# Kernel optimization log

Hardware: AMD Instinct MI355X
Metric: run time of the kernel (lower is better)

## Reference

```python
import jax, jax.numpy as jnp
import numpy as np

B, F, C = 16384, 256, 256


def setup_inputs() -> dict:
    key = jax.random.key(0)
    ks = jax.random.split(key, 10)
    return {
        "x_t": jax.random.normal(ks[0], (B, F), dtype=jnp.float32),
        "n_t": jax.random.normal(ks[1], (B, C), dtype=jnp.float32),
        "d_t": jax.random.uniform(ks[2], (B, C), dtype=jnp.float32),
        "h_t": jax.random.normal(ks[3], (B, C), dtype=jnp.float32),
        "a_max_t": jax.random.normal(ks[4], (B, C), dtype=jnp.float32),
        "Wu": jax.random.normal(ks[5], (C, F), dtype=jnp.float32) * 0.06,
        "bu": jnp.zeros((C,), dtype=jnp.float32),
        "Wg": jax.random.normal(ks[6], (C, F + C), dtype=jnp.float32) * 0.05,
        "bg": jnp.zeros((C,), dtype=jnp.float32),
        "Wa": jax.random.normal(ks[7], (C, F + C), dtype=jnp.float32) * 0.05,
        "Wd": jax.random.normal(ks[8], (C, F + C), dtype=jnp.float32) * 0.05,
    }


def reference(x_t, n_t, d_t, h_t, a_max_t, Wu, bu, Wg, bg, Wa, Wd):
    # xh_join = cat([x_t, h_t], dim=1) -> [B, F+C]
    xh = jnp.concatenate([x_t, h_t], axis=1)
    u_t = x_t @ Wu.T + bu                      # [B, C]
    g_t = xh @ Wg.T + bg                       # [B, C]
    a_t = xh @ Wa.T                            # [B, C] (no bias)
    z_t = u_t * jnp.tanh(g_t)
    # decay branch (self.decay is an nn.Linear -> always truthy in original)
    decay = jax.nn.sigmoid(xh @ Wd.T)
    e_neg = jnp.exp(-decay)
    a_decay = a_max_t * e_neg
    a_newmax = jnp.maximum(a_decay, a_t)
    exp_diff = jnp.exp(a_max_t - a_newmax)
    exp_scaled = jnp.exp(a_t - a_newmax)
    n_new = n_t * e_neg * exp_diff + z_t * exp_scaled
    d_new = d_t * e_neg * exp_diff + exp_scaled
    h_new = jnp.tanh(n_new / d_new)
    return (n_new, d_new, h_new, a_newmax)
```

## Files before the change

### kernel.cpp

```cpp
#include <hip/hip_runtime.h>
#include <stdint.h>

typedef _Float16 f16x8 __attribute__((ext_vector_type(8)));
typedef __fp16 fp16x2 __attribute__((ext_vector_type(2)));
typedef float f32x4 __attribute__((ext_vector_type(4)));

#define BC (16384 * 256)

__device__ __forceinline__ f16x8 cvt8(f32x4 a, f32x4 b) {
  fp16x2 p0 = __builtin_amdgcn_cvt_pkrtz(a[0], a[1]);
  fp16x2 p1 = __builtin_amdgcn_cvt_pkrtz(a[2], a[3]);
  fp16x2 p2 = __builtin_amdgcn_cvt_pkrtz(b[0], b[1]);
  fp16x2 p3 = __builtin_amdgcn_cvt_pkrtz(b[2], b[3]);
  f16x8 o;
  o[0] = (_Float16)p0[0]; o[1] = (_Float16)p0[1];
  o[2] = (_Float16)p1[0]; o[3] = (_Float16)p1[1];
  o[4] = (_Float16)p2[0]; o[5] = (_Float16)p2[1];
  o[6] = (_Float16)p3[0]; o[7] = (_Float16)p3[1];
  return o;
}

__device__ __forceinline__ float tanh_fast(float v) {
  float a = fminf(fabsf(v), 18.f);
  float t = __expf(2.f * a);
  float r = (t - 1.f) * __builtin_amdgcn_rcpf(t + 1.f);
  return copysignf(r, v);
}

__global__ __launch_bounds__(256) void pack_w(const float* __restrict__ Wu,
                                              const float* __restrict__ Wg,
                                              const float* __restrict__ Wa,
                                              const float* __restrict__ Wd,
                                              _Float16* __restrict__ wsB) {
  int tid = blockIdx.x * 256 + threadIdx.x;
  int slot = tid & 3;
  int row = (tid >> 2) & 127;
  int cb = (tid >> 9) & 7;
  int kt = tid >> 12;
  int strip = (row >> 4) & 3;
  int wn = row >> 6;
  int t16 = row & 15;
  int c = cb * 32 + wn * 16 + t16;
  int k0 = kt * 32 + (slot ^ ((row >> 1) & 3)) * 8;
  float v[8];
  if (strip == 0) {
    if (k0 < 256) {
      const float* p = Wu + (size_t)c * 256 + k0;
#pragma unroll
      for (int i = 0; i < 8; ++i) v[i] = p[i];
    } else {
#pragma unroll
      for (int i = 0; i < 8; ++i) v[i] = 0.f;
    }
  } else {
    const float* p = (strip == 1 ? Wg : (strip == 2 ? Wa : Wd)) + (size_t)c * 512 + k0;
#pragma unroll
    for (int i = 0; i < 8; ++i) v[i] = p[i];
  }
  f32x4 a = {v[0], v[1], v[2], v[3]};
  f32x4 b = {v[4], v[5], v[6], v[7]};
  *reinterpret_cast<f16x8*>(wsB + (size_t)tid * 8) = cvt8(a, b);
}

__global__ __launch_bounds__(256, 6) void rwa_main(
    const float* __restrict__ x, const float* __restrict__ nt_,
    const float* __restrict__ dt_, const float* __restrict__ h,
    const float* __restrict__ amax_, const float* __restrict__ bu,
    const float* __restrict__ bg, const _Float16* __restrict__ wsB,
    float* __restrict__ out) {
  __shared__ __align__(16) _Float16 ldsA[2][64 * 32];
  __shared__ __align__(16) _Float16 ldsB[2][128 * 32];

  const int tid = threadIdx.x;
  const int lane = tid & 63;
  const int l15 = lane & 15;
  const int lg = lane >> 4;
  const int wv = tid >> 6;
  const int wm = wv & 1;
  const int wn = wv >> 1;

  const int bid = blockIdx.x;
  const int xcd = bid & 7;
  const int q = bid >> 3;
  const int cb = q & 7;
  const int rowblk = xcd * 32 + (q >> 3);
  const int row0 = rowblk * 64;

  const int ar = tid >> 2;
  const int aq = tid & 3;
  const int awoff = ar * 64 + ((aq ^ ((ar >> 1) & 3)) << 4);

  const _Float16* bsrc0 = wsB + (size_t)cb * 4096 + (size_t)tid * 8;

  f32x4 acc[2][4] = {};
  f32x4 a0, a1;

  auto issueA = [&](int kt) {
    const float* sp = (kt < 8 ? x : h) + (size_t)(row0 + ar) * 256 + (kt & 7) * 32 + aq * 8;
    a0 = *reinterpret_cast<const f32x4*>(sp);
    a1 = *reinterpret_cast<const f32x4*>(sp + 4);
  };
  auto issueB = [&](int buf, int kt) {
#pragma unroll
    for (int i = 0; i < 2; ++i) {
      __builtin_amdgcn_global_load_lds(
          (const __attribute__((address_space(1))) uint32_t*)(bsrc0 + (size_t)kt * 32768 + i * 2048),
          (__attribute__((address_space(3))) uint32_t*)(&ldsB[buf][0] + wv * 512 + i * 2048),
          16, 0, 0);
    }
  };
  auto writeA = [&](int buf) {
    *reinterpret_cast<f16x8*>(reinterpret_cast<char*>(&ldsA[buf][0]) + awoff) = cvt8(a0, a1);
  };

  issueA(0);
  issueB(0, 0);
  writeA(0);

#pragma unroll
  for (int kt = 0; kt < 16; ++kt) {
    const int buf = kt & 1;
    if (kt < 15) {
      issueA(kt + 1);
      issueB(buf ^ 1, kt + 1);
    }

    if (kt < 15) {
      asm volatile("s_waitcnt vmcnt(4) lgkmcnt(0)" ::: "memory");
    } else {
      asm volatile("s_waitcnt vmcnt(0) lgkmcnt(0)" ::: "memory");
    }
    __builtin_amdgcn_s_barrier();
    __builtin_amdgcn_sched_barrier(0);

    const bool doU = (kt < 8);
    const char* pA = reinterpret_cast<const char*>(&ldsA[buf][0]);
    const char* pB = reinterpret_cast<const char*>(&ldsB[buf][0]);
    {
      f16x8 af[2], bf[4];
#pragma unroll
      for (int mi = 0; mi < 2; ++mi) {
        const int row = wm * 32 + mi * 16 + l15;
        af[mi] = *reinterpret_cast<const f16x8*>(pA + row * 64 + ((lg ^ ((row >> 1) & 3)) << 4));
      }
#pragma unroll
      for (int s = 0; s < 4; ++s) {
        if (s == 0 && !doU) continue;
        const int pc = wn * 64 + s * 16 + l15;
        bf[s] = *reinterpret_cast<const f16x8*>(pB + pc * 64 + ((lg ^ ((pc >> 1) & 3)) << 4));
      }
#pragma unroll
      for (int s = 0; s < 4; ++s) {
        if (s == 0 && !doU) continue;
#pragma unroll
        for (int mi = 0; mi < 2; ++mi)
          acc[mi][s] = __builtin_amdgcn_mfma_f32_16x16x32_f16(af[mi], bf[s], acc[mi][s], 0, 0, 0);
      }
    }

    if (kt < 15) {
      writeA(buf ^ 1);
      asm volatile("s_waitcnt lgkmcnt(0)" ::: "memory");
      __builtin_amdgcn_s_barrier();
      __builtin_amdgcn_sched_barrier(0);
    }
  }

  __builtin_amdgcn_sched_barrier(0);

  const int c = cb * 32 + wn * 16 + l15;
  const float buv = bu[c];
  const float bgv = bg[c];
#pragma unroll
  for (int mi = 0; mi < 2; ++mi) {
#pragma unroll
    for (int rg = 0; rg < 4; ++rg) {
      const int r = row0 + wm * 32 + mi * 16 + lg * 4 + rg;
      const int idx = r * 256 + c;
      const float u = acc[mi][0][rg] + buv;
      const float gt = acc[mi][1][rg] + bgv;
      const float a = acc[mi][2][rg];
      const float dr = acc[mi][3][rg];
      const float sig = __builtin_amdgcn_rcpf(1.f + __expf(-dr));
      const float z = u * tanh_fast(gt);
      const float am = amax_[idx];
      const float n_old = nt_[idx];
      const float d_old = dt_[idx];
      const float e_neg = __expf(-sig);
      const float a_new = fmaxf(am * e_neg, a);
      const float comm = __expf(am - a_new - sig);
      const float escal = __expf(a - a_new);
      const float n_new = n_old * comm + z * escal;
      const float d_new = d_old * comm + escal;
      const float h_new = tanh_fast(n_new * __builtin_amdgcn_rcpf(d_new));
      out[idx] = n_new;
      out[BC + idx] = d_new;
      out[2 * BC + idx] = h_new;
      out[3 * BC + idx] = a_new;
    }
  }
}

extern "C" void kernel_launch(void* const* d_in, const int* in_sizes, int n_in,
                              void* d_out, int out_size, void* d_ws, size_t ws_size,
                              hipStream_t stream) {
  const float* x_t    = (const float*)d_in[0];
  const float* n_t    = (const float*)d_in[1];
  const float* d_t    = (const float*)d_in[2];
  const float* h_t    = (const float*)d_in[3];
  const float* amax_t = (const float*)d_in[4];
  const float* Wu     = (const float*)d_in[5];
  const float* bu     = (const float*)d_in[6];
  const float* Wg     = (const float*)d_in[7];
  const float* bg     = (const float*)d_in[8];
  const float* Wa     = (const float*)d_in[9];
  const float* Wd     = (const float*)d_in[10];
  float* out = (float*)d_out;

  _Float16* wsB = (_Float16*)d_ws;

  pack_w<<<256, 256, 0, stream>>>(Wu, Wg, Wa, Wd, wsB);
  rwa_main<<<2048, 256, 0, stream>>>(x_t, n_t, d_t, h_t, amax_t, bu, bg, wsB, out);
}
```

Measured before the change: 46.52 us.

## Use single-wave blocks loading A fragments directly from global into registers

Restructures the main kernel from 4-wave 64x128 tiles to 1-wave blocks computing 32 rows by 16 output columns across all four gate strips. The activation fragments are now loaded straight from global memory into MFMA register layout, so the LDS staging for A and all block barriers go away. The packed weight layout is reordered to match. The cost is less reuse: each activation row is re-read by 16 column blocks instead of 8, and the grid grows to 8192 small blocks.

Measured after the change: 89.41 us. +92.2%, slower.

```diff
diff --git a/kernel.cpp b/kernel.cpp
--- a/kernel.cpp
+++ b/kernel.cpp
@@ -34,16 +34,14 @@
                                               _Float16* __restrict__ wsB) {
   int tid = blockIdx.x * 256 + threadIdx.x;
   int slot = tid & 3;
-  int row = (tid >> 2) & 127;
-  int cb = (tid >> 9) & 7;
-  int kt = tid >> 12;
-  int strip = (row >> 4) & 3;
-  int wn = row >> 6;
-  int t16 = row & 15;
-  int c = cb * 32 + wn * 16 + t16;
-  int k0 = kt * 32 + (slot ^ ((row >> 1) & 3)) * 8;
+  int pr = (tid >> 2) & 63;
+  int kt = (tid >> 8) & 15;
+  int cbh = tid >> 12;
+  int s = pr >> 4;
+  int c = cbh * 16 + (pr & 15);
+  int k0 = kt * 32 + (slot ^ ((pr >> 1) & 3)) * 8;
   float v[8];
-  if (strip == 0) {
+  if (s == 0) {
     if (k0 < 256) {
       const float* p = Wu + (size_t)c * 256 + k0;
 #pragma unroll
@@ -53,7 +51,7 @@
       for (int i = 0; i < 8; ++i) v[i] = 0.f;
     }
   } else {
-    const float* p = (strip == 1 ? Wg : (strip == 2 ? Wa : Wd)) + (size_t)c * 512 + k0;
+    const float* p = (s == 1 ? Wg : (s == 2 ? Wa : Wd)) + (size_t)c * 512 + k0;
 #pragma unroll
     for (int i = 0; i < 8; ++i) v[i] = p[i];
   }
@@ -62,120 +60,102 @@
   *reinterpret_cast<f16x8*>(wsB + (size_t)tid * 8) = cvt8(a, b);
 }
 
-__global__ __launch_bounds__(256, 6) void rwa_main(
+__global__ __launch_bounds__(64, 4) void rwa_main(
     const float* __restrict__ x, const float* __restrict__ nt_,
     const float* __restrict__ dt_, const float* __restrict__ h,
     const float* __restrict__ amax_, const float* __restrict__ bu,
     const float* __restrict__ bg, const _Float16* __restrict__ wsB,
     float* __restrict__ out) {
-  __shared__ __align__(16) _Float16 ldsA[2][64 * 32];
-  __shared__ __align__(16) _Float16 ldsB[2][128 * 32];
-
-  const int tid = threadIdx.x;
-  const int lane = tid & 63;
+  __shared__ __align__(16) _Float16 ldsB[2][64 * 32];
+
+  const int lane = threadIdx.x;
   const int l15 = lane & 15;
   const int lg = lane >> 4;
-  const int wv = tid >> 6;
-  const int wm = wv & 1;
-  const int wn = wv >> 1;
 
   const int bid = blockIdx.x;
   const int xcd = bid & 7;
   const int q = bid >> 3;
-  const int cb = q & 7;
-  const int rowblk = xcd * 32 + (q >> 3);
-  const int row0 = rowblk * 64;
-
-  const int ar = tid >> 2;
-  const int aq = tid & 3;
-  const int awoff = ar * 64 + ((aq ^ ((ar >> 1) & 3)) << 4);
-
-  const _Float16* bsrc0 = wsB + (size_t)cb * 4096 + (size_t)tid * 8;
+  const int cbh = q & 15;
+  const int r32 = xcd * 64 + (q >> 4);
+  const int row0 = r32 * 32;
+
+  const float* xr0 = x + (size_t)(row0 + l15) * 256 + lg * 8;
+  const float* hr0 = h + (size_t)(row0 + l15) * 256 + lg * 8;
+  const float* xr1 = xr0 + 16 * 256;
+  const float* hr1 = hr0 + 16 * 256;
+
+  const _Float16* bslab = wsB + (size_t)cbh * 32768 + (size_t)lane * 8;
 
   f32x4 acc[2][4] = {};
-  f32x4 a0, a1;
+  f32x4 a0, a1, a2, a3;
 
   auto issueA = [&](int kt) {
-    const float* sp = (kt < 8 ? x : h) + (size_t)(row0 + ar) * 256 + (kt & 7) * 32 + aq * 8;
-    a0 = *reinterpret_cast<const f32x4*>(sp);
-    a1 = *reinterpret_cast<const f32x4*>(sp + 4);
+    const float* p0 = (kt < 8 ? xr0 : hr0) + (kt & 7) * 32;
+    const float* p1 = (kt < 8 ? xr1 : hr1) + (kt & 7) * 32;
+    a0 = *reinterpret_cast<const f32x4*>(p0);
+    a1 = *reinterpret_cast<const f32x4*>(p0 + 4);
+    a2 = *reinterpret_cast<const f32x4*>(p1);
+    a3 = *reinterpret_cast<const f32x4*>(p1 + 4);
   };
   auto issueB = [&](int buf, int kt) {
 #pragma unroll
-    for (int i = 0; i < 2; ++i) {
+    for (int i = 0; i < 4; ++i) {
       __builtin_amdgcn_global_load_lds(
-          (const __attribute__((address_space(1))) uint32_t*)(bsrc0 + (size_t)kt * 32768 + i * 2048),
-          (__attribute__((address_space(3))) uint32_t*)(&ldsB[buf][0] + wv * 512 + i * 2048),
+          (const __attribute__((address_space(1))) uint32_t*)(bslab + (size_t)kt * 2048 + i * 512),
+          (__attribute__((address_space(3))) uint32_t*)(&ldsB[buf][0] + i * 512),
           16, 0, 0);
     }
-  };
-  auto writeA = [&](int buf) {
-    *reinterpret_cast<f16x8*>(reinterpret_cast<char*>(&ldsA[buf][0]) + awoff) = cvt8(a0, a1);
   };
 
   issueA(0);
   issueB(0, 0);
-  writeA(0);
 
 #pragma unroll
   for (int kt = 0; kt < 16; ++kt) {
     const int buf = kt & 1;
+
+    f16x8 af0 = cvt8(a0, a1);
+    f16x8 af1 = cvt8(a2, a3);
+
     if (kt < 15) {
       issueA(kt + 1);
       issueB(buf ^ 1, kt + 1);
     }
 
     if (kt < 15) {
-      asm volatile("s_waitcnt vmcnt(4) lgkmcnt(0)" ::: "memory");
+      asm volatile("s_waitcnt vmcnt(8)" ::: "memory");
     } else {
-      asm volatile("s_waitcnt vmcnt(0) lgkmcnt(0)" ::: "memory");
-    }
-    __builtin_amdgcn_s_barrier();
+      asm volatile("s_waitcnt vmcnt(0)" ::: "memory");
+    }
     __builtin_amdgcn_sched_barrier(0);
 
     const bool doU = (kt < 8);
-    const char* pA = reinterpret_cast<const char*>(&ldsA[buf][0]);
     const char* pB = reinterpret_cast<const char*>(&ldsB[buf][0]);
-    {
-      f16x8 af[2], bf[4];
-#pragma unroll
-      for (int mi = 0; mi < 2; ++mi) {
-        const int row = wm * 32 + mi * 16 + l15;
-        af[mi] = *reinterpret_cast<const f16x8*>(pA + row * 64 + ((lg ^ ((row >> 1) & 3)) << 4));
-      }
-#pragma unroll
-      for (int s = 0; s < 4; ++s) {
-        if (s == 0 && !doU) continue;
-        const int pc = wn * 64 + s * 16 + l15;
-        bf[s] = *reinterpret_cast<const f16x8*>(pB + pc * 64 + ((lg ^ ((pc >> 1) & 3)) << 4));
-      }
-#pragma unroll
-      for (int s = 0; s < 4; ++s) {
-        if (s == 0 && !doU) continue;
-#pragma unroll
-        for (int mi = 0; mi < 2; ++mi)
-          acc[mi][s] = __builtin_amdgcn_mfma_f32_16x16x32_f16(af[mi], bf[s], acc[mi][s], 0, 0, 0);
-      }
-    }
-
-    if (kt < 15) {
-      writeA(buf ^ 1);
-      asm volatile("s_waitcnt lgkmcnt(0)" ::: "memory");
-      __builtin_amdgcn_s_barrier();
-      __builtin_amdgcn_sched_barrier(0);
+    f16x8 bf[4];
+#pragma unroll
+    for (int s = 0; s < 4; ++s) {
+      if (s == 0 && !doU) continue;
+      const int pr = s * 16 + l15;
+      bf[s] = *reinterpret_cast<const f16x8*>(pB + pr * 64 + ((lg ^ ((pr >> 1) & 3)) << 4));
+    }
+#pragma unroll
+    for (int s = 0; s < 4; ++s) {
+      if (s == 0 && !doU) continue;
+      acc[0][s] = __builtin_amdgcn_mfma_f32_16x16x32_f16(af0, bf[s], acc[0][s], 0, 0, 0);
+      acc[1][s] = __builtin_amdgcn_mfma_f32_16x16x32_f16(af1, bf[s], acc[1][s], 0, 0, 0);
     }
   }
 
   __builtin_amdgcn_sched_barrier(0);
 
-  const int c = cb * 32 + wn * 16 + l15;
+  const int c = cbh * 16 + l15;
   const float buv = bu[c];
   const float bgv = bg[c];
 #pragma unroll
   for (int mi = 0; mi < 2; ++mi) {
 #pragma unroll
     for (int rg = 0; rg < 4; ++rg) {
-      const int r = row0 + wm * 32 + mi * 16 + lg * 4 + rg;
+      const int r = row0 + mi * 16 + lg * 4 + rg;
       const int idx = r * 256 + c;
       const float u = acc[mi][0][rg] + buv;
       const float gt = acc[mi][1][rg] + bgv;
@@ -220,5 +200,5 @@
   _Float16* wsB = (_Float16*)d_ws;
 
   pack_w<<<256, 256, 0, stream>>>(Wu, Wg, Wa, Wd, wsB);
-  rwa_main<<<2048, 256, 0, stream>>>(x_t, n_t, d_t, h_t, amax_t, bu, bg, wsB, out);
-}
+  rwa_main<<<8192, 64, 0, stream>>>(x_t, n_t, d_t, h_t, amax_t, bu, bg, wsB, out);
+}
```
